# Optimization experiments

Hardware: AMD Instinct MI355X
Metric: run time of the kernel (lower is better)

Reference implementation:

```python
import jax, jax.numpy as jnp
import numpy as np

N_QUBITS = 12
RANK = 1024
K = 4            # outcomes per qubit
D = 2 ** N_QUBITS
N_IDX = 1_000_000


def setup_inputs() -> dict:
    key = jax.random.key(0)
    k1, k2, k3, k4 = jax.random.split(key, 4)
    params = jax.random.normal(k1, (2, D, RANK), dtype=jnp.float32)
    M_real = jax.random.normal(k2, (K, 2, 2), dtype=jnp.float32)
    M_imag = jax.random.normal(k3, (K, 2, 2), dtype=jnp.float32)
    P_idxs = jax.random.randint(k4, (N_IDX,), 0, K ** N_QUBITS, dtype=jnp.int64)
    return {"params": params, "M_real": M_real, "M_imag": M_imag, "P_idxs": P_idxs}


def _qmt(rho, M, n_qubits):
    """Born rule: P[s1..sN] = Tr[(M_{s1} x ... x M_{sN}) rho].
    Sequential per-qubit contraction; T has shape [K^n, 2^(N-n), 2^(N-n)]."""
    T = rho[None, :, :]  # axes: (done outcomes, row legs j, col legs i)
    for _ in range(n_qubits):
        k, r, c = T.shape[0], T.shape[1] // 2, T.shape[2] // 2
        Tt = T.reshape(k, 2, r, 2, c)  # (k, j_n, j_rest, i_n, i_rest)
        # Tr contribution: sum_{i,j} M[s,i,j] * rho[j,i]
        T = jnp.einsum('sij,kjait->ksat', M, Tt).reshape(k * M.shape[0], r, c)
    return T.reshape(-1)  # [K^N] complex


def reference(params, M_real, M_imag, P_idxs):
    # rho = U U^H / Tr(U U^H)
    U = jax.lax.complex(params[0], params[1])            # [D, RANK] complex64
    rho = U @ U.conj().T                                  # [D, D]
    rho = rho / jnp.trace(rho)
    M = jax.lax.complex(M_real, M_imag)                   # [K, 2, 2] complex64
    P_all = _qmt(rho, M, N_QUBITS).real                   # [K^N] float32
    return P_all[P_idxs]
```

## Files before the change

kernel.cpp:

```cpp
#include <hip/hip_runtime.h>

#define D 4096
#define RANK 1024
#define K2 2048
#define UELEMS 4194304ULL
#define NTOT 16777216ULL
#define QSCALE 16000.0f

typedef __attribute__((ext_vector_type(4))) int i32x4;

__device__ float g_inv_tr[1];
__device__ float g_scale[D];
__device__ float g_mdre[16];
__device__ float g_mdim[16];

static __device__ __forceinline__ void load_lds16(const void* g, void* l) {
    __builtin_amdgcn_global_load_lds(
        (const __attribute__((address_space(1))) unsigned int*)g,
        (__attribute__((address_space(3))) unsigned int*)l, 16, 0, 0);
}

__global__ __launch_bounds__(256) void convert_w_i8(const float* __restrict__ P,
                                                    const float* __restrict__ Mre,
                                                    const float* __restrict__ Mim,
                                                    char* __restrict__ Wh,
                                                    char* __restrict__ Wl,
                                                    char* __restrict__ N2h,
                                                    char* __restrict__ N2l)
{
    if (blockIdx.x == 0 && threadIdx.x < 16) {
        const int s = threadIdx.x >> 2, i = (threadIdx.x >> 1) & 1, j = threadIdx.x & 1;
        g_mdre[threadIdx.x] =  Mre[s * 4 + j * 2 + i];
        g_mdim[threadIdx.x] = -Mim[s * 4 + j * 2 + i];
    }

    const int w = threadIdx.x >> 6, lane = threadIdx.x & 63;
    const int row = blockIdx.x * 4 + w;

    float ur[16], ui[16];
    const float* pr = P + (size_t)row * RANK + lane * 16;
    const float* pi = P + UELEMS + (size_t)row * RANK + lane * 16;
    #pragma unroll
    for (int q = 0; q < 4; ++q) {
        const float4 a = ((const float4*)pr)[q];
        const float4 b = ((const float4*)pi)[q];
        ur[q * 4 + 0] = a.x; ur[q * 4 + 1] = a.y; ur[q * 4 + 2] = a.z; ur[q * 4 + 3] = a.w;
        ui[q * 4 + 0] = b.x; ui[q * 4 + 1] = b.y; ui[q * 4 + 2] = b.z; ui[q * 4 + 3] = b.w;
    }
    float mx = 0.f;
    #pragma unroll
    for (int e = 0; e < 16; ++e)
        mx = fmaxf(mx, fmaxf(fabsf(ur[e]), fabsf(ui[e])));
    #pragma unroll
    for (int off = 1; off < 64; off <<= 1)
        mx = fmaxf(mx, __shfl_xor(mx, off));
    const float inv = mx > 0.f ? QSCALE / mx : 0.f;
    if (lane == 0) g_scale[row] = mx / QSCALE;

    int hr[16], lr[16], hi[16], li[16];
    #pragma unroll
    for (int e = 0; e < 16; ++e) {
        float q = ur[e] * inv;
        float hf = rintf(q * 0.0078125f);
        hr[e] = (int)hf; lr[e] = (int)rintf(q - 128.f * hf);
        q = ui[e] * inv;
        hf = rintf(q * 0.0078125f);
        hi[e] = (int)hf; li[e] = (int)rintf(q - 128.f * hf);
    }
    uint4 phr, plr, phi, pli, pnh, pnl;
    unsigned* dst[6] = {(unsigned*)&phr, (unsigned*)&plr, (unsigned*)&phi,
                        (unsigned*)&pli, (unsigned*)&pnh, (unsigned*)&pnl};
    #pragma unroll
    for (int q = 0; q < 4; ++q) {
        unsigned a = 0, b = 0, c = 0, d = 0, e = 0, f = 0;
        #pragma unroll
        for (int k = 0; k < 4; ++k) {
            const int sh = k * 8;
            a |= (unsigned)(hr[q * 4 + k] & 255) << sh;
            b |= (unsigned)(lr[q * 4 + k] & 255) << sh;
            c |= (unsigned)(hi[q * 4 + k] & 255) << sh;
            d |= (unsigned)(li[q * 4 + k] & 255) << sh;
            e |= (unsigned)((-hi[q * 4 + k]) & 255) << sh;
            f |= (unsigned)((-li[q * 4 + k]) & 255) << sh;
        }
        dst[0][q] = a; dst[1][q] = b; dst[2][q] = c; dst[3][q] = d; dst[4][q] = e; dst[5][q] = f;
    }
    const size_t b1 = (size_t)row * 2048 + lane * 16;
    *(uint4*)&Wh[b1] = phr;          *(uint4*)&Wl[b1] = plr;
    *(uint4*)&Wh[b1 + 1024] = phi;   *(uint4*)&Wl[b1 + 1024] = pli;
    const size_t b2 = (size_t)row * 1024 + lane * 16;
    *(uint4*)&N2h[b2] = pnh;         *(uint4*)&N2l[b2] = pnl;
}

__global__ __launch_bounds__(256, 2) void gemm_rho_i8(const char* __restrict__ Wh,
                                                      const char* __restrict__ Wl,
                                                      const char* __restrict__ N2h,
                                                      const char* __restrict__ N2l,
                                                      float2* __restrict__ rho)
{
    __shared__ __align__(16) char sA1h[64 * 64];
    __shared__ __align__(16) char sA1l[64 * 64];
    __shared__ __align__(16) char sA2h[64 * 64];
    __shared__ __align__(16) char sA2l[64 * 64];
    __shared__ __align__(16) char sB1h[128 * 64];
    __shared__ __align__(16) char sB1l[128 * 64];
    __shared__ __align__(16) char sB2h[128 * 64];
    __shared__ __align__(16) char sB2l[128 * 64];
    __shared__ __align__(16) char sN2h[128 * 64];
    __shared__ __align__(16) char sN2l[128 * 64];

    const int b = blockIdx.x;
    int bj = (int)((65.0f - sqrtf(4225.0f - 4.0f * (float)b)) * 0.5f);
    while (bj > 0 && bj * (65 - bj) > b) --bj;
    while ((bj + 1) * (64 - bj) <= b) ++bj;
    const int bi = 2 * bj + (b - bj * (65 - bj));
    const int row0 = bi << 6, col0 = bj << 7;
    const bool full = (bi >= 2 * bj + 2);

    const int t = threadIdx.x;
    const int lane = t & 63, w = t >> 6;
    const int wr = w >> 1, wc = w & 1;

    const int rowA = t >> 2;
    const int kcA = (t & 3) ^ ((rowA >> 1) & 3);
    const size_t aoff = (size_t)(row0 + rowA) * 2048 + kcA * 16;
    const int ldsA = t * 16;
    size_t boff[2], boffN[2]; int ldsB[2];
    #pragma unroll
    for (int q = 0; q < 2; ++q) {
        const int g = q * 256 + t;
        const int rowB = g >> 2;
        const int kcB = (g & 3) ^ ((rowB >> 1) & 3);
        boff[q]  = (size_t)(col0 + rowB) * 2048 + kcB * 16;
        boffN[q] = (size_t)(col0 + rowB) * 1024 + kcB * 16;
        ldsB[q] = g * 16;
    }

    const int m = lane & 15, gq = lane >> 4;
    const int fko = (gq ^ ((m >> 1) & 3)) * 16;

    i32x4 rehh[2][4], remx[2][4], imhh[2][4], immx[2][4];
    #pragma unroll
    for (int i = 0; i < 2; ++i)
        #pragma unroll
        for (int j = 0; j < 4; ++j) {
            rehh[i][j] = (i32x4){0, 0, 0, 0}; remx[i][j] = (i32x4){0, 0, 0, 0};
            imhh[i][j] = (i32x4){0, 0, 0, 0}; immx[i][j] = (i32x4){0, 0, 0, 0};
        }

    for (int kt = 0; kt < RANK; kt += 64) {
        load_lds16(Wh + aoff + kt,        &sA1h[ldsA]);
        load_lds16(Wl + aoff + kt,        &sA1l[ldsA]);
        load_lds16(Wh + aoff + kt + 1024, &sA2h[ldsA]);
        load_lds16(Wl + aoff + kt + 1024, &sA2l[ldsA]);
        #pragma unroll
        for (int q = 0; q < 2; ++q) {
            load_lds16(Wh + boff[q] + kt,        &sB1h[ldsB[q]]);
            load_lds16(Wl + boff[q] + kt,        &sB1l[ldsB[q]]);
            load_lds16(Wh + boff[q] + kt + 1024, &sB2h[ldsB[q]]);
            load_lds16(Wl + boff[q] + kt + 1024, &sB2l[ldsB[q]]);
            load_lds16(N2h + boffN[q] + kt,      &sN2h[ldsB[q]]);
            load_lds16(N2l + boffN[q] + kt,      &sN2l[ldsB[q]]);
        }
        __syncthreads();

        i32x4 fa1h[2], fa1l[2], fa2h[2], fa2l[2];
        #pragma unroll
        for (int i = 0; i < 2; ++i) {
            const int off = (wr * 32 + i * 16 + m) * 64 + fko;
            fa1h[i] = *(const i32x4*)&sA1h[off];
            fa1l[i] = *(const i32x4*)&sA1l[off];
            fa2h[i] = *(const i32x4*)&sA2h[off];
            fa2l[i] = *(const i32x4*)&sA2l[off];
        }
        #pragma unroll
        for (int j = 0; j < 4; ++j) {
            const int off = (wc * 64 + j * 16 + m) * 64 + fko;
            const i32x4 b1h = *(const i32x4*)&sB1h[off];
            const i32x4 b1l = *(const i32x4*)&sB1l[off];
            const i32x4 b2h = *(const i32x4*)&sB2h[off];
            const i32x4 b2l = *(const i32x4*)&sB2l[off];
            const i32x4 n2h = *(const i32x4*)&sN2h[off];
            const i32x4 n2l = *(const i32x4*)&sN2l[off];
            #pragma unroll
            for (int i = 0; i < 2; ++i) {
                i32x4 r = rehh[i][j];
                r = __builtin_amdgcn_mfma_i32_16x16x64_i8(fa1h[i], b1h, r, 0, 0, 0);
                r = __builtin_amdgcn_mfma_i32_16x16x64_i8(fa2h[i], b2h, r, 0, 0, 0);
                rehh[i][j] = r;
                r = remx[i][j];
                r = __builtin_amdgcn_mfma_i32_16x16x64_i8(fa1h[i], b1l, r, 0, 0, 0);
                r = __builtin_amdgcn_mfma_i32_16x16x64_i8(fa1l[i], b1h, r, 0, 0, 0);
                r = __builtin_amdgcn_mfma_i32_16x16x64_i8(fa2h[i], b2l, r, 0, 0, 0);
                r = __builtin_amdgcn_mfma_i32_16x16x64_i8(fa2l[i], b2h, r, 0, 0, 0);
                remx[i][j] = r;
                r = imhh[i][j];
                r = __builtin_amdgcn_mfma_i32_16x16x64_i8(fa2h[i], b1h, r, 0, 0, 0);
                r = __builtin_amdgcn_mfma_i32_16x16x64_i8(fa1h[i], n2h, r, 0, 0, 0);
                imhh[i][j] = r;
                r = immx[i][j];
                r = __builtin_amdgcn_mfma_i32_16x16x64_i8(fa2h[i], b1l, r, 0, 0, 0);
                r = __builtin_amdgcn_mfma_i32_16x16x64_i8(fa2l[i], b1h, r, 0, 0, 0);
                r = __builtin_amdgcn_mfma_i32_16x16x64_i8(fa1h[i], n2l, r, 0, 0, 0);
                r = __builtin_amdgcn_mfma_i32_16x16x64_i8(fa1l[i], n2h, r, 0, 0, 0);
                immx[i][j] = r;
            }
        }
        __syncthreads();
    }

    #pragma unroll
    for (int i = 0; i < 2; ++i)
        #pragma unroll
        for (int j = 0; j < 4; ++j) {
            const int col = col0 + wc * 64 + j * 16 + m;
            const float sc = g_scale[col];
            #pragma unroll
            for (int r = 0; r < 4; ++r) {
                const int row = row0 + wr * 32 + i * 16 + gq * 4 + r;
                const float s2 = g_scale[row] * sc;
                const float re = s2 * (16384.f * (float)rehh[i][j][r] + 128.f * (float)remx[i][j][r]);
                const float im = s2 * (16384.f * (float)imhh[i][j][r] + 128.f * (float)immx[i][j][r]);
                if (full || row >= col) rho[(size_t)row * D + col] = make_float2(re, im);
                if (row > col && ((row >> 6) == (col >> 6)))
                    rho[(size_t)col * D + row] = make_float2(re, -im);
            }
        }
}

__global__ void trace_inv(const float2* __restrict__ rho)
{
    __shared__ float red[256];
    float s = 0.f;
    for (int d = threadIdx.x; d < D; d += 256)
        s += rho[(size_t)d * (D + 1)].x;
    red[threadIdx.x] = s;
    __syncthreads();
    for (int off = 128; off > 0; off >>= 1) {
        if (threadIdx.x < off) red[threadIdx.x] += red[threadIdx.x + off];
        __syncthreads();
    }
    if (threadIdx.x == 0) g_inv_tr[0] = 1.0f / red[0];
}

static __device__ __forceinline__ void qmt2(float2* x,
                                            const float* __restrict__ Mre,
                                            const float* __restrict__ Mim)
{
    float2 y[16];
    #pragma unroll
    for (int sb = 0; sb < 4; ++sb)
        #pragma unroll
        for (int ja = 0; ja < 2; ++ja)
            #pragma unroll
            for (int ia = 0; ia < 2; ++ia) {
                float2 acc = make_float2(0.f, 0.f);
                #pragma unroll
                for (int ib = 0; ib < 2; ++ib)
                    #pragma unroll
                    for (int jb = 0; jb < 2; ++jb) {
                        const float mr = Mre[sb * 4 + ib * 2 + jb];
                        const float mi = Mim[sb * 4 + ib * 2 + jb];
                        const float2 v = x[(ja * 2 + jb) * 4 + ia * 2 + ib];
                        acc.x += mr * v.x - mi * v.y;
                        acc.y += mr * v.y + mi * v.x;
                    }
                y[sb * 4 + ja * 2 + ia] = acc;
            }
    #pragma unroll
    for (int sa = 0; sa < 4; ++sa)
        #pragma unroll
        for (int sb = 0; sb < 4; ++sb) {
            float2 acc = make_float2(0.f, 0.f);
            #pragma unroll
            for (int ia = 0; ia < 2; ++ia)
                #pragma unroll
                for (int ja = 0; ja < 2; ++ja) {
                    const float mr = Mre[sa * 4 + ia * 2 + ja];
                    const float mi = Mim[sa * 4 + ia * 2 + ja];
                    const float2 v = y[sb * 4 + ja * 2 + ia];
                    acc.x += mr * v.x - mi * v.y;
                    acc.y += mr * v.y + mi * v.x;
                }
            x[sa * 4 + sb] = acc;
        }
}

static __device__ __forceinline__ void pA_pipeline(float2* x, float2* X, const int t,
                                                   const float* __restrict__ mre,
                                                   const float* __restrict__ mim)
{
    qmt2(x, mre, mim);
    #pragma unroll
    for (int d = 0; d < 16; ++d) X[t * 17 + d] = x[d];
    __syncthreads();
    const int a2 = t >> 6, t2 = (t >> 4) & 3, d1 = t & 15;
    #pragma unroll
    for (int j2 = 0; j2 < 4; ++j2)
        #pragma unroll
        for (int i2 = 0; i2 < 4; ++i2)
            x[j2 * 4 + i2] = X[((a2 * 4 + j2) * 16 + t2 * 4 + i2) * 17 + d1];
    __syncthreads();
    qmt2(x, mre, mim);
    #pragma unroll
    for (int d = 0; d < 16; ++d) X[(a2 * 4 + t2) * 257 + d * 16 + d1] = x[d];
    __syncthreads();
    const int e2 = t >> 4, e1 = t & 15;
    #pragma unroll
    for (int j2 = 0; j2 < 4; ++j2)
        #pragma unroll
        for (int i2 = 0; i2 < 4; ++i2)
            x[j2 * 4 + i2] = X[(j2 * 4 + i2) * 257 + e2 * 16 + e1];
    qmt2(x, mre, mim);
}

__global__ __launch_bounds__(256) void qmt_pAh(const float2* __restrict__ in,
                                               float2* __restrict__ out,
                                               const float* __restrict__ Mre,
                                               const float* __restrict__ Mim)
{
    __shared__ __align__(16) float2 X[256 * 17];
    const int t = threadIdx.x;
    const int g = blockIdx.x;
    int rr = (int)((sqrtf(8.f * (float)g + 1.f) - 1.f) * 0.5f);
    while (rr * (rr + 1) / 2 > g) --rr;
    while ((rr + 1) * (rr + 2) / 2 <= g) ++rr;
    const int cc = g - rr * (rr + 1) / 2;

    const int a4 = t >> 4, t4 = t & 15;
    float2 x0[16], x[16];
    #pragma unroll
    for (int j2 = 0; j2 < 4; ++j2) {
        const float2* p = in + ((size_t)(rr * 64 + a4 * 4 + j2)) * 4096 + cc * 64 + t4 * 4;
        const float4 v0 = ((const float4*)p)[0];
        const float4 v1 = ((const float4*)p)[1];
        x0[j2 * 4 + 0] = make_float2(v0.x, v0.y);
        x0[j2 * 4 + 1] = make_float2(v0.z, v0.w);
        x0[j2 * 4 + 2] = make_float2(v1.x, v1.y);
        x0[j2 * 4 + 3] = make_float2(v1.z, v1.w);
    }

    #pragma unroll
    for (int q = 0; q < 16; ++q) x[q] = x0[q];
    pA_pipeline(x, X, t, Mre, Mim);
    const int e2 = t >> 4, e1 = t & 15;
    const size_t ob0 = (size_t)(rr * 64 + cc) * 4096 + e2 * 16 + e1;
    #pragma unroll
    for (int d = 0; d < 16; ++d) out[ob0 + (size_t)d * 256] = x[d];

    if (rr != cc) {
        __syncthreads();
        #pragma unroll
        for (int q = 0; q < 16; ++q) x[q] = x0[q];
        pA_pipeline(x, X, t, g_mdre, g_mdim);
        const size_t ob1 = (size_t)(cc * 64 + rr) * 4096 + e2 * 16 + e1;
        #pragma unroll
        for (int d = 0; d < 16; ++d)
            out[ob1 + (size_t)d * 256] = make_float2(x[d].x, -x[d].y);
    }
}

static __device__ __forceinline__ void qmt_stage_cb(float2* x,
                                                    const float* __restrict__ Mre,
                                                    const float* __restrict__ Mim)
{
    #pragma unroll
    for (int jj = 0; jj < 4; ++jj) {
        float2 y[16];
        #pragma unroll
        for (int sc = 0; sc < 4; ++sc)
            #pragma unroll
            for (int ii = 0; ii < 4; ++ii) {
                float2 acc = make_float2(0.f, 0.f);
                #pragma unroll
                for (int ic = 0; ic < 2; ++ic)
                    #pragma unroll
                    for (int jc = 0; jc < 2; ++jc) {
                        const float mr = Mre[sc * 4 + ic * 2 + jc];
                        const float mi = Mim[sc * 4 + ic * 2 + jc];
                        const float2 v = x[jj * 16 + jc * 8 + ii * 2 + ic];
                        acc.x += mr * v.x - mi * v.y;
                        acc.y += mr * v.y + mi * v.x;
                    }
                y[sc * 4 + ii] = acc;
            }
        #pragma unroll
        for (int q = 0; q < 16; ++q) x[jj * 16 + q] = y[q];
    }

    #pragma unroll
    for (int ja = 0; ja < 2; ++ja)
        #pragma unroll
        for (int sc = 0; sc < 4; ++sc) {
            float2 z[8];
            #pragma unroll
            for (int sb = 0; sb < 4; ++sb)
                #pragma unroll
                for (int ia = 0; ia < 2; ++ia) {
                    float2 acc = make_float2(0.f, 0.f);
                    #pragma unroll
                    for (int ib = 0; ib < 2; ++ib)
                        #pragma unroll
                        for (int jb = 0; jb < 2; ++jb) {
                            const float mr = Mre[sb * 4 + ib * 2 + jb];
                            const float mi = Mim[sb * 4 + ib * 2 + jb];
                            const float2 v = x[(ja * 2 + jb) * 16 + sc * 4 + ia * 2 + ib];
                            acc.x += mr * v.x - mi * v.y;
                            acc.y += mr * v.y + mi * v.x;
                        }
                    z[sb * 2 + ia] = acc;
                }
            #pragma unroll
            for (int sb = 0; sb < 4; ++sb)
                #pragma unroll
                for (int ia = 0; ia < 2; ++ia)
                    x[ja * 32 + (sb >> 1) * 16 + sc * 4 + ia * 2 + (sb & 1)] = z[sb * 2 + ia];
        }
}

#define QMT_STAGE_A(STORE)                                                     \
    _Pragma("unroll")                                                          \
    for (int sbH = 0; sbH < 2; ++sbH)                                          \
        _Pragma("unroll")                                                      \
        for (int sc = 0; sc < 4; ++sc)                                         \
            _Pragma("unroll")                                                  \
            for (int sbL = 0; sbL < 2; ++sbL) {                                \
                const int sb = sbH * 2 + sbL;                                  \
                _Pragma("unroll")                                              \
                for (int sa = 0; sa < 4; ++sa) {                               \
                    float2 acc = make_float2(0.f, 0.f);                        \
                    _Pragma("unroll")                                          \
                    for (int ia = 0; ia < 2; ++ia)                             \
                        _Pragma("unroll")                                      \
                        for (int ja = 0; ja < 2; ++ja) {                       \
                            const float mr = Mre[sa * 4 + ia * 2 + ja];        \
                            const float mi = Mim[sa * 4 + ia * 2 + ja];        \
                            const float2 v = x[ja * 32 + sbH * 16 + sc * 4 + ia * 2 + sbL]; \
                            acc.x += mr * v.x - mi * v.y;                      \
                            acc.y += mr * v.y + mi * v.x;                      \
                        }                                                      \
                    const int s3 = sa * 16 + sb * 4 + sc;                      \
                    STORE;                                                     \
                }                                                              \
            }

__global__ __launch_bounds__(256) void qmt_p3(const float2* __restrict__ in,
                                              float2* __restrict__ out,
                                              const float* __restrict__ Mre,
                                              const float* __restrict__ Mim)
{
    const int tid = blockIdx.x * 256 + threadIdx.x;
    const int s = tid & 4095, c3 = (tid >> 12) & 7, r3 = tid >> 15;

    float2 x[64];
    #pragma unroll
    for (int j3 = 0; j3 < 8; ++j3)
        #pragma unroll
        for (int i3 = 0; i3 < 8; ++i3)
            x[j3 * 8 + i3] = in[(size_t)((r3 * 8 + j3) * 64 + c3 * 8 + i3) * 4096 + s];
    qmt_stage_cb(x, Mre, Mim);
    const size_t ob = ((size_t)(r3 * 8 + c3) * 64) * 4096 + s;
    QMT_STAGE_A(out[ob + s3 * 4096] = acc)
}

__global__ __launch_bounds__(256) void qmt_p4(const float2* __restrict__ in,
                                              float* __restrict__ out,
                                              const float* __restrict__ Mre,
                                              const float* __restrict__ Mim)
{
    const int tid = blockIdx.x * 256 + threadIdx.x;
    float2 x[64];
    #pragma unroll
    for (int j3 = 0; j3 < 8; ++j3)
        #pragma unroll
        for (int i3 = 0; i3 < 8; ++i3)
            x[j3 * 8 + i3] = in[(size_t)(j3 * 8 + i3) * 262144 + tid];
    qmt_stage_cb(x, Mre, Mim);
    const size_t ob = (size_t)(tid >> 5) * 2048 + (tid & 31);
    QMT_STAGE_A(out[ob + s3 * 32] = acc.x)
}

__global__ void gather_idx(const float* __restrict__ P, const int* __restrict__ idxs,
                           float* __restrict__ out, const int n)
{
    const int i = blockIdx.x * 256 + threadIdx.x;
    if (i < n) {
        const int idx = idxs[i];
        const int s = idx & 262143;
        const size_t pos = (size_t)(s >> 5) * 2048 + (size_t)(idx >> 18) * 32 + (s & 31);
        out[i] = P[pos] * g_inv_tr[0];
    }
}

extern "C" void kernel_launch(void* const* d_in, const int* in_sizes, int n_in,
                              void* d_out, int out_size, void* d_ws, size_t ws_size,
                              hipStream_t stream)
{
    const float* params = (const float*)d_in[0];
    const float* Mre    = (const float*)d_in[1];
    const float* Mim    = (const float*)d_in[2];
    const int*   idxs   = (const int*)d_in[3];
    float*       out    = (float*)d_out;

    float* ws = (float*)d_ws;
    float2* A  = (float2*)ws;
    float2* Bp = (float2*)(ws + 2 * NTOT);
    char* Wh  = (char*)Bp;
    char* Wl  = Wh + (size_t)D * 2048;
    char* N2h = Wl + (size_t)D * 2048;
    char* N2l = N2h + (size_t)D * 1024;

    convert_w_i8<<<1024, 256, 0, stream>>>(params, Mre, Mim, Wh, Wl, N2h, N2l);
    gemm_rho_i8<<<1056, 256, 0, stream>>>(Wh, Wl, N2h, N2l, A);
    trace_inv<<<1, 256, 0, stream>>>(A);

    qmt_pAh<<<2080, 256, 0, stream>>>(A, Bp, Mre, Mim);
    qmt_p3<<<1024, 256, 0, stream>>>(Bp, A, Mre, Mim);
    qmt_p4<<<1024, 256, 0, stream>>>(A, (float*)Bp, Mre, Mim);

    gather_idx<<<(out_size + 255) / 256, 256, 0, stream>>>((float*)Bp, idxs, out, out_size);
}
```

Measured before the change: 433.7 us.

## Fuse int8 rho GEMM epilogue with first QMT stage and trace accumulation

The GEMM epilogue now stages each 64x64 rho tile in shared memory and applies the first QMT pipeline directly, writing both the tile and its Hermitian mirror. This removes the full rho round trip through global memory and the separate qmt_pAh kernel. The single-block trace kernel is replaced by per-wave atomic accumulation of diagonal entries into g_tr, which convert_w_i8 zeroes at the start. In exchange, shared memory is reused as a 64 KB pool, the epilogue gains extra barriers and register pressure, and the trace sum now depends on atomic ordering.

```diff
diff --git a/kernel.cpp b/kernel.cpp
--- a/kernel.cpp
+++ b/kernel.cpp
@@ -9,7 +9,7 @@
 
 typedef __attribute__((ext_vector_type(4))) int i32x4;
 
-__device__ float g_inv_tr[1];
+__device__ float g_tr[1];
 __device__ float g_scale[D];
 __device__ float g_mdre[16];
 __device__ float g_mdim[16];
@@ -28,10 +28,13 @@
                                                     char* __restrict__ N2h,
                                                     char* __restrict__ N2l)
 {
-    if (blockIdx.x == 0 && threadIdx.x < 16) {
-        const int s = threadIdx.x >> 2, i = (threadIdx.x >> 1) & 1, j = threadIdx.x & 1;
-        g_mdre[threadIdx.x] =  Mre[s * 4 + j * 2 + i];
-        g_mdim[threadIdx.x] = -Mim[s * 4 + j * 2 + i];
+    if (blockIdx.x == 0) {
+        if (threadIdx.x < 16) {
+            const int s = threadIdx.x >> 2, i = (threadIdx.x >> 1) & 1, j = threadIdx.x & 1;
+            g_mdre[threadIdx.x] =  Mre[s * 4 + j * 2 + i];
+            g_mdim[threadIdx.x] = -Mim[s * 4 + j * 2 + i];
+        }
+        if (threadIdx.x == 16) g_tr[0] = 0.f;
     }
 
     const int w = threadIdx.x >> 6, lane = threadIdx.x & 63;
@@ -92,22 +95,96 @@
     *(uint4*)&N2h[b2] = pnh;         *(uint4*)&N2l[b2] = pnl;
 }
 
-__global__ __launch_bounds__(256, 2) void gemm_rho_i8(const char* __restrict__ Wh,
-                                                      const char* __restrict__ Wl,
-                                                      const char* __restrict__ N2h,
-                                                      const char* __restrict__ N2l,
-                                                      float2* __restrict__ rho)
-{
-    __shared__ __align__(16) char sA1h[64 * 64];
-    __shared__ __align__(16) char sA1l[64 * 64];
-    __shared__ __align__(16) char sA2h[64 * 64];
-    __shared__ __align__(16) char sA2l[64 * 64];
-    __shared__ __align__(16) char sB1h[128 * 64];
-    __shared__ __align__(16) char sB1l[128 * 64];
-    __shared__ __align__(16) char sB2h[128 * 64];
-    __shared__ __align__(16) char sB2l[128 * 64];
-    __shared__ __align__(16) char sN2h[128 * 64];
-    __shared__ __align__(16) char sN2l[128 * 64];
+static __device__ __forceinline__ void qmt2(float2* x,
+                                            const float* __restrict__ Mre,
+                                            const float* __restrict__ Mim)
+{
+    float2 y[16];
+    #pragma unroll
+    for (int sb = 0; sb < 4; ++sb)
+        #pragma unroll
+        for (int ja = 0; ja < 2; ++ja)
+            #pragma unroll
+            for (int ia = 0; ia < 2; ++ia) {
+                float2 acc = make_float2(0.f, 0.f);
+                #pragma unroll
+                for (int ib = 0; ib < 2; ++ib)
+                    #pragma unroll
+                    for (int jb = 0; jb < 2; ++jb) {
+                        const float mr = Mre[sb * 4 + ib * 2 + jb];
+                        const float mi = Mim[sb * 4 + ib * 2 + jb];
+                        const float2 v = x[(ja * 2 + jb) * 4 + ia * 2 + ib];
+                        acc.x += mr * v.x - mi * v.y;
+                        acc.y += mr * v.y + mi * v.x;
+                    }
+                y[sb * 4 + ja * 2 + ia] = acc;
+            }
+    #pragma unroll
+    for (int sa = 0; sa < 4; ++sa)
+        #pragma unroll
+        for (int sb = 0; sb < 4; ++sb) {
+            float2 acc = make_float2(0.f, 0.f);
+            #pragma unroll
+            for (int ia = 0; ia < 2; ++ia)
+                #pragma unroll
+                for (int ja = 0; ja < 2; ++ja) {
+                    const float mr = Mre[sa * 4 + ia * 2 + ja];
+                    const float mi = Mim[sa * 4 + ia * 2 + ja];
+                    const float2 v = y[sb * 4 + ja * 2 + ia];
+                    acc.x += mr * v.x - mi * v.y;
+                    acc.y += mr * v.y + mi * v.x;
+                }
+            x[sa * 4 + sb] = acc;
+        }
+}
+
+static __device__ __forceinline__ void pA_pipeline(float2* x, float2* X, const int t,
+                                                   const float* __restrict__ mre,
+                                                   const float* __restrict__ mim)
+{
+    qmt2(x, mre, mim);
+    #pragma unroll
+    for (int d = 0; d < 16; ++d) X[t * 17 + d] = x[d];
+    __syncthreads();
+    const int a2 = t >> 6, t2 = (t >> 4) & 3, d1 = t & 15;
+    #pragma unroll
+    for (int j2 = 0; j2 < 4; ++j2)
+        #pragma unroll
+        for (int i2 = 0; i2 < 4; ++i2)
+            x[j2 * 4 + i2] = X[((a2 * 4 + j2) * 16 + t2 * 4 + i2) * 17 + d1];
+    __syncthreads();
+    qmt2(x, mre, mim);
+    #pragma unroll
+    for (int d = 0; d < 16; ++d) X[(a2 * 4 + t2) * 257 + d * 16 + d1] = x[d];
+    __syncthreads();
+    const int e2 = t >> 4, e1 = t & 15;
+    #pragma unroll
+    for (int j2 = 0; j2 < 4; ++j2)
+        #pragma unroll
+        for (int i2 = 0; i2 < 4; ++i2)
+            x[j2 * 4 + i2] = X[(j2 * 4 + i2) * 257 + e2 * 16 + e1];
+    qmt2(x, mre, mim);
+}
+
+__global__ __launch_bounds__(256, 2) void gemm_qmtA(const char* __restrict__ Wh,
+                                                    const char* __restrict__ Wl,
+                                                    const char* __restrict__ N2h,
+                                                    const char* __restrict__ N2l,
+                                                    const float* __restrict__ Mre,
+                                                    const float* __restrict__ Mim,
+                                                    float2* __restrict__ out)
+{
+    __shared__ __align__(16) char pool[65536];
+    char* const sA1h = pool;
+    char* const sA1l = pool + 4096;
+    char* const sA2h = pool + 8192;
+    char* const sA2l = pool + 12288;
+    char* const sB1h = pool + 16384;
+    char* const sB1l = pool + 24576;
+    char* const sB2h = pool + 32768;
+    char* const sB2l = pool + 40960;
+    char* const sN2h = pool + 49152;
+    char* const sN2l = pool + 57344;
 
     const int b = blockIdx.x;
     int bj = (int)((65.0f - sqrtf(4225.0f - 4.0f * (float)b)) * 0.5f);
@@ -115,7 +192,6 @@
     while ((bj + 1) * (64 - bj) <= b) ++bj;
     const int bi = 2 * bj + (b - bj * (65 - bj));
     const int row0 = bi << 6, col0 = bj << 7;
-    const bool full = (bi >= 2 * bj + 2);
 
     const int t = threadIdx.x;
     const int lane = t & 63, w = t >> 6;
@@ -149,18 +225,18 @@
         }
 
     for (int kt = 0; kt < RANK; kt += 64) {
-        load_lds16(Wh + aoff + kt,        &sA1h[ldsA]);
-        load_lds16(Wl + aoff + kt,        &sA1l[ldsA]);
-        load_lds16(Wh + aoff + kt + 1024, &sA2h[ldsA]);
-        load_lds16(Wl + aoff + kt + 1024, &sA2l[ldsA]);
+        load_lds16(Wh + aoff + kt,        sA1h + ldsA);
+        load_lds16(Wl + aoff + kt,        sA1l + ldsA);
+        load_lds16(Wh + aoff + kt + 1024, sA2h + ldsA);
+        load_lds16(Wl + aoff + kt + 1024, sA2l + ldsA);
         #pragma unroll
         for (int q = 0; q < 2; ++q) {
-            load_lds16(Wh + boff[q] + kt,        &sB1h[ldsB[q]]);
-            load_lds16(Wl + boff[q] + kt,        &sB1l[ldsB[q]]);
-            load_lds16(Wh + boff[q] + kt + 1024, &sB2h[ldsB[q]]);
-            load_lds16(Wl + boff[q] + kt + 1024, &sB2l[ldsB[q]]);
-            load_lds16(N2h + boffN[q] + kt,      &sN2h[ldsB[q]]);
-            load_lds16(N2l + boffN[q] + kt,      &sN2l[ldsB[q]]);
+            load_lds16(Wh + boff[q] + kt,        sB1h + ldsB[q]);
+            load_lds16(Wl + boff[q] + kt,        sB1l + ldsB[q]);
+            load_lds16(Wh + boff[q] + kt + 1024, sB2h + ldsB[q]);
+            load_lds16(Wl + boff[q] + kt + 1024, sB2l + ldsB[q]);
+            load_lds16(N2h + boffN[q] + kt,      sN2h + ldsB[q]);
+            load_lds16(N2l + boffN[q] + kt,      sN2l + ldsB[q]);
         }
         __syncthreads();
 
@@ -209,155 +285,73 @@
         __syncthreads();
     }
 
-    #pragma unroll
-    for (int i = 0; i < 2; ++i)
-        #pragma unroll
-        for (int j = 0; j < 4; ++j) {
-            const int col = col0 + wc * 64 + j * 16 + m;
-            const float sc = g_scale[col];
-            #pragma unroll
-            for (int r = 0; r < 4; ++r) {
-                const int row = row0 + wr * 32 + i * 16 + gq * 4 + r;
-                const float s2 = g_scale[row] * sc;
-                const float re = s2 * (16384.f * (float)rehh[i][j][r] + 128.f * (float)remx[i][j][r]);
-                const float im = s2 * (16384.f * (float)imhh[i][j][r] + 128.f * (float)immx[i][j][r]);
-                if (full || row >= col) rho[(size_t)row * D + col] = make_float2(re, im);
-                if (row > col && ((row >> 6) == (col >> 6)))
-                    rho[(size_t)col * D + row] = make_float2(re, -im);
-            }
-        }
-}
-
-__global__ void trace_inv(const float2* __restrict__ rho)
-{
-    __shared__ float red[256];
-    float s = 0.f;
-    for (int d = threadIdx.x; d < D; d += 256)
-        s += rho[(size_t)d * (D + 1)].x;
-    red[threadIdx.x] = s;
-    __syncthreads();
-    for (int off = 128; off > 0; off >>= 1) {
-        if (threadIdx.x < off) red[threadIdx.x] += red[threadIdx.x + off];
+    float2* const Tile = (float2*)pool;
+    float2* const X    = (float2*)pool;
+    float trloc = 0.f;
+    const int e2 = t >> 4, e1 = t & 15;
+    const int a4 = t >> 4, t4 = t & 15;
+
+    #pragma unroll
+    for (int h = 0; h < 2; ++h) {
+        const int ccT = 2 * bj + h;
+        if (ccT > bi) continue;
+        const bool diag = (ccT == bi);
+
+        if (wc == h) {
+            #pragma unroll
+            for (int i = 0; i < 2; ++i)
+                #pragma unroll
+                for (int j = 0; j < 4; ++j) {
+                    const int col_l = j * 16 + m;
+                    const float sc = g_scale[ccT * 64 + col_l];
+                    #pragma unroll
+                    for (int r = 0; r < 4; ++r) {
+                        const int row_l = wr * 32 + i * 16 + gq * 4 + r;
+                        const float s2 = g_scale[row0 + row_l] * sc;
+                        const float re = s2 * (16384.f * (float)rehh[i][j][r] + 128.f * (float)remx[i][j][r]);
+                        const float im = s2 * (16384.f * (float)imhh[i][j][r] + 128.f * (float)immx[i][j][r]);
+                        Tile[row_l * 66 + col_l] = make_float2(re, im);
+                        if (diag && row_l == col_l) trloc += re;
+                    }
+                }
+        }
         __syncthreads();
-    }
-    if (threadIdx.x == 0) g_inv_tr[0] = 1.0f / red[0];
-}
-
-static __device__ __forceinline__ void qmt2(float2* x,
-                                            const float* __restrict__ Mre,
-                                            const float* __restrict__ Mim)
-{
-    float2 y[16];
-    #pragma unroll
-    for (int sb = 0; sb < 4; ++sb)
-        #pragma unroll
-        for (int ja = 0; ja < 2; ++ja)
-            #pragma unroll
-            for (int ia = 0; ia < 2; ++ia) {
-                float2 acc = make_float2(0.f, 0.f);
-                #pragma unroll
-                for (int ib = 0; ib < 2; ++ib)
-                    #pragma unroll
-                    for (int jb = 0; jb < 2; ++jb) {
-                        const float mr = Mre[sb * 4 + ib * 2 + jb];
-                        const float mi = Mim[sb * 4 + ib * 2 + jb];
-                        const float2 v = x[(ja * 2 + jb) * 4 + ia * 2 + ib];
-                        acc.x += mr * v.x - mi * v.y;
-                        acc.y += mr * v.y + mi * v.x;
-                    }
-                y[sb * 4 + ja * 2 + ia] = acc;
-            }
-    #pragma unroll
-    for (int sa = 0; sa < 4; ++sa)
-        #pragma unroll
-        for (int sb = 0; sb < 4; ++sb) {
-            float2 acc = make_float2(0.f, 0.f);
-            #pragma unroll
-            for (int ia = 0; ia < 2; ++ia)
-                #pragma unroll
-                for (int ja = 0; ja < 2; ++ja) {
-                    const float mr = Mre[sa * 4 + ia * 2 + ja];
-                    const float mi = Mim[sa * 4 + ia * 2 + ja];
-                    const float2 v = y[sb * 4 + ja * 2 + ia];
-                    acc.x += mr * v.x - mi * v.y;
-                    acc.y += mr * v.y + mi * v.x;
-                }
-            x[sa * 4 + sb] = acc;
-        }
-}
-
-static __device__ __forceinline__ void pA_pipeline(float2* x, float2* X, const int t,
-                                                   const float* __restrict__ mre,
-                                                   const float* __restrict__ mim)
-{
-    qmt2(x, mre, mim);
-    #pragma unroll
-    for (int d = 0; d < 16; ++d) X[t * 17 + d] = x[d];
-    __syncthreads();
-    const int a2 = t >> 6, t2 = (t >> 4) & 3, d1 = t & 15;
-    #pragma unroll
-    for (int j2 = 0; j2 < 4; ++j2)
-        #pragma unroll
-        for (int i2 = 0; i2 < 4; ++i2)
-            x[j2 * 4 + i2] = X[((a2 * 4 + j2) * 16 + t2 * 4 + i2) * 17 + d1];
-    __syncthreads();
-    qmt2(x, mre, mim);
-    #pragma unroll
-    for (int d = 0; d < 16; ++d) X[(a2 * 4 + t2) * 257 + d * 16 + d1] = x[d];
-    __syncthreads();
-    const int e2 = t >> 4, e1 = t & 15;
-    #pragma unroll
-    for (int j2 = 0; j2 < 4; ++j2)
-        #pragma unroll
-        for (int i2 = 0; i2 < 4; ++i2)
-            x[j2 * 4 + i2] = X[(j2 * 4 + i2) * 257 + e2 * 16 + e1];
-    qmt2(x, mre, mim);
-}
-
-__global__ __launch_bounds__(256) void qmt_pAh(const float2* __restrict__ in,
-                                               float2* __restrict__ out,
-                                               const float* __restrict__ Mre,
-                                               const float* __restrict__ Mim)
-{
-    __shared__ __align__(16) float2 X[256 * 17];
-    const int t = threadIdx.x;
-    const int g = blockIdx.x;
-    int rr = (int)((sqrtf(8.f * (float)g + 1.f) - 1.f) * 0.5f);
-    while (rr * (rr + 1) / 2 > g) --rr;
-    while ((rr + 1) * (rr + 2) / 2 <= g) ++rr;
-    const int cc = g - rr * (rr + 1) / 2;
-
-    const int a4 = t >> 4, t4 = t & 15;
-    float2 x0[16], x[16];
-    #pragma unroll
-    for (int j2 = 0; j2 < 4; ++j2) {
-        const float2* p = in + ((size_t)(rr * 64 + a4 * 4 + j2)) * 4096 + cc * 64 + t4 * 4;
-        const float4 v0 = ((const float4*)p)[0];
-        const float4 v1 = ((const float4*)p)[1];
-        x0[j2 * 4 + 0] = make_float2(v0.x, v0.y);
-        x0[j2 * 4 + 1] = make_float2(v0.z, v0.w);
-        x0[j2 * 4 + 2] = make_float2(v1.x, v1.y);
-        x0[j2 * 4 + 3] = make_float2(v1.z, v1.w);
-    }
-
-    #pragma unroll
-    for (int q = 0; q < 16; ++q) x[q] = x0[q];
-    pA_pipeline(x, X, t, Mre, Mim);
-    const int e2 = t >> 4, e1 = t & 15;
-    const size_t ob0 = (size_t)(rr * 64 + cc) * 4096 + e2 * 16 + e1;
-    #pragma unroll
-    for (int d = 0; d < 16; ++d) out[ob0 + (size_t)d * 256] = x[d];
-
-    if (rr != cc) {
+
+        float2 x0[16], x[16];
+        #pragma unroll
+        for (int j2 = 0; j2 < 4; ++j2) {
+            const float4* p = (const float4*)&Tile[(a4 * 4 + j2) * 66 + t4 * 4];
+            const float4 v0 = p[0], v1 = p[1];
+            x0[j2 * 4 + 0] = make_float2(v0.x, v0.y);
+            x0[j2 * 4 + 1] = make_float2(v0.z, v0.w);
+            x0[j2 * 4 + 2] = make_float2(v1.x, v1.y);
+            x0[j2 * 4 + 3] = make_float2(v1.z, v1.w);
+        }
         __syncthreads();
+
         #pragma unroll
         for (int q = 0; q < 16; ++q) x[q] = x0[q];
-        pA_pipeline(x, X, t, g_mdre, g_mdim);
-        const size_t ob1 = (size_t)(cc * 64 + rr) * 4096 + e2 * 16 + e1;
-        #pragma unroll
-        for (int d = 0; d < 16; ++d)
-            out[ob1 + (size_t)d * 256] = make_float2(x[d].x, -x[d].y);
-    }
+        pA_pipeline(x, X, t, Mre, Mim);
+        const size_t ob0 = (size_t)(bi * 64 + ccT) * 4096 + e2 * 16 + e1;
+        #pragma unroll
+        for (int d = 0; d < 16; ++d) out[ob0 + (size_t)d * 256] = x[d];
+
+        if (!diag) {
+            __syncthreads();
+            #pragma unroll
+            for (int q = 0; q < 16; ++q) x[q] = x0[q];
+            pA_pipeline(x, X, t, g_mdre, g_mdim);
+            const size_t ob1 = (size_t)(ccT * 64 + bi) * 4096 + e2 * 16 + e1;
+            #pragma unroll
+            for (int d = 0; d < 16; ++d)
+                out[ob1 + (size_t)d * 256] = make_float2(x[d].x, -x[d].y);
+        }
+        __syncthreads();
+    }
+
+    #pragma unroll
+    for (int off = 1; off < 64; off <<= 1) trloc += __shfl_xor(trloc, off);
+    if (lane == 0 && trloc != 0.f) atomicAdd(&g_tr[0], trloc);
 }
 
 static __device__ __forceinline__ void qmt_stage_cb(float2* x,
@@ -488,7 +482,7 @@
         const int idx = idxs[i];
         const int s = idx & 262143;
         const size_t pos = (size_t)(s >> 5) * 2048 + (size_t)(idx >> 18) * 32 + (s & 31);
-        out[i] = P[pos] * g_inv_tr[0];
+        out[i] = P[pos] * (1.0f / g_tr[0]);
     }
 }
 
@@ -511,12 +505,9 @@
     char* N2l = N2h + (size_t)D * 1024;
 
     convert_w_i8<<<1024, 256, 0, stream>>>(params, Mre, Mim, Wh, Wl, N2h, N2l);
-    gemm_rho_i8<<<1056, 256, 0, stream>>>(Wh, Wl, N2h, N2l, A);
-    trace_inv<<<1, 256, 0, stream>>>(A);
-
-    qmt_pAh<<<2080, 256, 0, stream>>>(A, Bp, Mre, Mim);
-    qmt_p3<<<1024, 256, 0, stream>>>(Bp, A, Mre, Mim);
-    qmt_p4<<<1024, 256, 0, stream>>>(A, (float*)Bp, Mre, Mim);
-
-    gather_idx<<<(out_size + 255) / 256, 256, 0, stream>>>((float*)Bp, idxs, out, out_size);
-}
+    gemm_qmtA<<<1056, 256, 0, stream>>>(Wh, Wl, N2h, N2l, Mre, Mim, A);
+    qmt_p3<<<1024, 256, 0, stream>>>(A, Bp, Mre, Mim);
+    qmt_p4<<<1024, 256, 0, stream>>>(Bp, (float*)A, Mre, Mim);
+
+    gather_idx<<<(out_size + 255) / 256, 256, 0, stream>>>((float*)A, idxs, out, out_size);
+}
```

After: 691.8 us. 1.6x slower.
